# Kernel tuning notes

Measured on AMD Instinct MI355X. Metric: run time of the kernel, lower is better.

## Reference

```python
import jax, jax.numpy as jnp
import numpy as np

N, D, E, L, NL = 100000, 64, 400000, 4, 10000
NEG = jnp.float32(-1e30)


def _make_graph(key):
    k1, k2, k3, k4 = jax.random.split(key, 4)
    ncov = N - NL
    # nodes [0, NL) never appear as source -> exactly NL leaves
    src_cov = jnp.arange(ncov, dtype=jnp.int32) + NL
    src_rand = jax.random.randint(k1, (E - ncov,), NL, N, dtype=jnp.int32)
    src = jnp.concatenate([src_cov, src_rand])
    dst = jax.random.randint(k2, (E,), 0, N, dtype=jnp.int32)
    edge_index = jnp.stack([src, dst])  # [2, E]
    edge_attr = jax.random.normal(k3, (E, D), jnp.float32)
    # partition edges into L 'topological level' masks
    edge_masks = (jnp.arange(E) % L)[None, :] == jnp.arange(L)[:, None]  # [L, E] bool
    x = jax.random.normal(k4, (N, D), jnp.float32)
    return x, edge_index, edge_attr, edge_masks


def setup_inputs() -> dict:
    key = jax.random.key(0)
    kg1, kg2, kp = jax.random.split(key, 3)
    x1, ei1, ea1, em1 = _make_graph(kg1)
    x2, ei2, ea2, em2 = _make_graph(kg2)
    ks = jax.random.split(kp, 10)
    s = 1.0 / np.sqrt(D)
    params = {
        'We': jax.random.normal(ks[0], (D, D), jnp.float32) * s,
        'be': jax.random.normal(ks[1], (D,), jnp.float32) * s,
        'Wa': jax.random.normal(ks[2], (1, 2 * D), jnp.float32) * s,
        'ba': jax.random.normal(ks[3], (1,), jnp.float32) * s,
        'Wih': jax.random.normal(ks[4], (3 * D, D), jnp.float32) * s,
        'Whh': jax.random.normal(ks[5], (3 * D, D), jnp.float32) * s,
        'bih': jax.random.normal(ks[6], (3 * D,), jnp.float32) * s,
        'bhh': jax.random.normal(ks[7], (3 * D,), jnp.float32) * s,
        'Wc': jax.random.normal(ks[8], (2 * D, 2 * D), jnp.float32) * s,
        'bc': jax.random.normal(ks[9], (2 * D,), jnp.float32) * s,
    }
    return dict(x1=x1, edge_index1=ei1, edge_attr1=ea1, edge_masks1=em1,
                x2=x2, edge_index2=ei2, edge_attr2=ea2, edge_masks2=em2,
                **params, n_leaf=NL)


def _gru(x, h, Wih, Whh, bih, bhh):
    # torch.nn.GRUCell math
    gi = x @ Wih.T + bih
    gh = h @ Whh.T + bhh
    ir, iz, in_ = jnp.split(gi, 3, axis=-1)
    hr, hz, hn = jnp.split(gh, 3, axis=-1)
    r = jax.nn.sigmoid(ir + hr)
    z = jax.nn.sigmoid(iz + hz)
    n = jnp.tanh(in_ + r * hn)
    return (1.0 - z) * n + z * h


def _flow_forward(x, edge_index, edge_attr, edge_masks,
                  We, be, Wa, ba, Wih, Whh, bih, bhh):
    Nn, Dm = x.shape
    src, dst = edge_index[0], edge_index[1]
    root = jnp.ones((Nn,), bool).at[dst].set(False)  # nodes with no incoming edge
    eemb = edge_attr @ We.T + be                     # [E, D] edge_lin
    # roots: GRU with zero hidden; others start at 0 (zeros_like in torch)
    h0 = jnp.where(root[:, None], _gru(x, jnp.zeros_like(x), Wih, Whh, bih, bhh), 0.0)
    q = x[dst]                                       # h_prev_i, level-invariant

    def step(h, mask):
        k = h[src] + eemb                            # h_j + edge_emb
        logit = (jnp.concatenate([q, k], axis=-1) @ Wa.T + ba)[:, 0]  # [E]
        ml = jnp.where(mask, logit, NEG)
        mx = jnp.maximum(jax.ops.segment_max(ml, dst, num_segments=Nn), NEG)
        ex = jnp.where(mask, jnp.exp(ml - mx[dst]), 0.0)  # scatter-softmax numerator
        den = jax.ops.segment_sum(ex, dst, num_segments=Nn)
        alpha = ex / (den[dst] + 1e-16)
        msg = jax.ops.segment_sum(alpha[:, None] * h[src], dst, num_segments=Nn)
        nm = jax.ops.segment_sum(mask.astype(jnp.float32), dst, num_segments=Nn) > 0
        h_new = _gru(x, msg, Wih, Whh, bih, bhh)     # input=h_prev, hidden=msg
        return jnp.where(nm[:, None], h_new, h), None

    h, _ = jax.lax.scan(step, h0, edge_masks)
    return h


def reference(x1, edge_index1, edge_attr1, edge_masks1,
              x2, edge_index2, edge_attr2, edge_masks2,
              We, be, Wa, ba, Wih, Whh, bih, bhh, Wc, bc, n_leaf):
    o1 = _flow_forward(x1, edge_index1, edge_attr1, edge_masks1,
                       We, be, Wa, ba, Wih, Whh, bih, bhh)
    o2 = _flow_forward(x2, edge_index2, edge_attr2, edge_masks2,
                       We, be, Wa, ba, Wih, Whh, bih, bhh)
    Dm = x1.shape[1]
    leaf1 = jnp.ones((x1.shape[0],), bool).at[edge_index1[0]].set(False)
    leaf2 = jnp.ones((x2.shape[0],), bool).at[edge_index2[0]].set(False)
    idx1 = jnp.nonzero(leaf1, size=n_leaf)[0]
    idx2 = jnp.nonzero(leaf2, size=n_leaf)[0]
    feat = jnp.concatenate([o1[idx1], o2[idx2]], axis=-1) @ Wc.T + bc  # [NL, 2D]
    o1 = o1.at[idx1].set(feat[:, :Dm])
    o2 = o2.at[idx2].set(feat[:, Dm:])
    return (o1, o2)
```

## Files before the change

### kernel.cpp

```cpp
#include <hip/hip_runtime.h>

#define NN 100000
#define DD 64
#define EE 400000
#define LL 4
#define NLEAF 10000
#define NT (2*NN)
#define ETOT (2*EE)
#define M4 (4*NT)
#define NBLK ((M4 + 1023)/1024)

typedef __attribute__((ext_vector_type(8))) short bf8v;
typedef __attribute__((ext_vector_type(4))) float f4v;
typedef __attribute__((ext_vector_type(8))) unsigned short su8;

__device__ __forceinline__ float rcp_(float x){ return __builtin_amdgcn_rcpf(x); }
__device__ __forceinline__ float sigm_(float x){ return rcp_(1.f + __expf(-x)); }
__device__ __forceinline__ float tanh_(float x){
  x = fminf(fmaxf(x, -15.f), 15.f);
  float a = __expf(2.f*x);
  return (a - 1.f) * rcp_(a + 1.f);
}
__device__ __forceinline__ float wave_sum(float p){
  #pragma unroll
  for (int m = 1; m < 64; m <<= 1) p += __shfl_xor(p, m, 64);
  return p;
}
__device__ __forceinline__ unsigned short f2b(float f){
  union { float f; unsigned int u; } v; v.f = f;
  unsigned int r = v.u + 0x7FFF + ((v.u >> 16) & 1);
  return (unsigned short)(r >> 16);
}
__device__ __forceinline__ float b2f(unsigned short b){
  union { unsigned int u; float f; } v; v.u = ((unsigned int)b) << 16;
  return v.f;
}
__device__ __forceinline__ int cnt_at(const unsigned int* pcnt, int i){
  int l = i / NT; int td = i - l*NT;
  return (int)((pcnt[td] >> (8*l)) & 255u);
}

__global__ void k_init(unsigned int* __restrict__ pcnt, int* __restrict__ wlcnt,
                       int* __restrict__ row_ptr,
                       float* __restrict__ vvec, float* __restrict__ c0v,
                       unsigned short* __restrict__ whh_bf,
                       unsigned short* __restrict__ wih_bf,
                       const float* __restrict__ We, const float* __restrict__ Wa,
                       const float* __restrict__ be, const float* __restrict__ Whh,
                       const float* __restrict__ Wih) {
  int tid = blockIdx.x*blockDim.x + threadIdx.x;
  int stride = gridDim.x*blockDim.x;
  for (int i = tid; i < NT; i += stride) pcnt[i] = 0u;
  for (int i = tid; i < 192*64; i += stride) whh_bf[i] = f2b(Whh[i]);
  for (int i = tid; i < 208*64; i += stride) {
    int n = i >> 6, k = i & 63;
    unsigned short v;
    if (n < 192)       v = f2b(Wih[i]);
    else if (n == 192) v = f2b(Wa[k]);
    else               v = 0;
    wih_bf[i] = v;
  }
  if (blockIdx.x == 0 && threadIdx.x < 64) {
    int c = threadIdx.x;
    float acc = 0.f;
    for (int d = 0; d < 64; ++d) acc += We[d*64 + c] * Wa[64 + d];
    vvec[c] = acc;
    float p = wave_sum(be[c] * Wa[64 + c]);
    if (c == 0) { c0v[0] = p; row_ptr[M4] = ETOT; }
    if (c < 8) wlcnt[c] = 0;
  }
}

__global__ __launch_bounds__(256) void k_edot(
    const float* __restrict__ ea1, const float* __restrict__ ea2,
    const int* __restrict__ ei1, const int* __restrict__ ei2,
    const float* __restrict__ vvec, const float* __restrict__ c0v,
    float* __restrict__ edot, unsigned int* __restrict__ pcnt,
    unsigned char* __restrict__ rank8) {
  int lane = threadIdx.x & 63;
  int wave = blockIdx.x*(blockDim.x>>6) + (threadIdx.x>>6);
  int nw = gridDim.x*(blockDim.x>>6);
  int grp = lane >> 4, l16 = lane & 15;
  float4 v4 = ((const float4*)vvec)[l16];
  float c0 = c0v[0];
  const int NIT = ETOT/16;
  for (int it = wave; it < NIT; it += 2*nw) {
    int it2 = it + nw;
    bool hasB = (it2 < NIT);
    int e0 = it*16 + grp;
    int g = e0 >= EE;
    const float* ea = g ? ea2 : ea1;
    long eb = e0 - (long)g*EE;
    float4 a0 = ((const float4*)(ea + (eb     )*64))[l16];
    float4 a1 = ((const float4*)(ea + (eb +  4)*64))[l16];
    float4 a2 = ((const float4*)(ea + (eb +  8)*64))[l16];
    float4 a3 = ((const float4*)(ea + (eb + 12)*64))[l16];
    float4 b0, b1, b2, b3; int e1 = 0;
    if (hasB) {
      e1 = it2*16 + grp;
      int g2 = e1 >= EE;
      const float* eb2 = g2 ? ea2 : ea1;
      long ebb = e1 - (long)g2*EE;
      b0 = ((const float4*)(eb2 + (ebb     )*64))[l16];
      b1 = ((const float4*)(eb2 + (ebb +  4)*64))[l16];
      b2 = ((const float4*)(eb2 + (ebb +  8)*64))[l16];
      b3 = ((const float4*)(eb2 + (ebb + 12)*64))[l16];
    } else {
      b0 = b1 = b2 = b3 = make_float4(0.f,0.f,0.f,0.f);
    }
    float p0 = a0.x*v4.x + a0.y*v4.y + a0.z*v4.z + a0.w*v4.w;
    float p1 = a1.x*v4.x + a1.y*v4.y + a1.z*v4.z + a1.w*v4.w;
    float p2 = a2.x*v4.x + a2.y*v4.y + a2.z*v4.z + a2.w*v4.w;
    float p3 = a3.x*v4.x + a3.y*v4.y + a3.z*v4.z + a3.w*v4.w;
    float q0 = b0.x*v4.x + b0.y*v4.y + b0.z*v4.z + b0.w*v4.w;
    float q1 = b1.x*v4.x + b1.y*v4.y + b1.z*v4.z + b1.w*v4.w;
    float q2 = b2.x*v4.x + b2.y*v4.y + b2.z*v4.z + b2.w*v4.w;
    float q3 = b3.x*v4.x + b3.y*v4.y + b3.z*v4.z + b3.w*v4.w;
    #pragma unroll
    for (int m = 1; m < 16; m <<= 1) {
      p0 += __shfl_xor(p0, m, 64); p1 += __shfl_xor(p1, m, 64);
      p2 += __shfl_xor(p2, m, 64); p3 += __shfl_xor(p3, m, 64);
      q0 += __shfl_xor(q0, m, 64); q1 += __shfl_xor(q1, m, 64);
      q2 += __shfl_xor(q2, m, 64); q3 += __shfl_xor(q3, m, 64);
    }
    if (l16 == 0) {
      edot[e0]      = p0 + c0;
      edot[e0 +  4] = p1 + c0;
      edot[e0 +  8] = p2 + c0;
      edot[e0 + 12] = p3 + c0;
      if (hasB) {
        edot[e1]      = q0 + c0;
        edot[e1 +  4] = q1 + c0;
        edot[e1 +  8] = q2 + c0;
        edot[e1 + 12] = q3 + c0;
      }
    }
  }
  int tid = blockIdx.x*blockDim.x + threadIdx.x;
  int stride = gridDim.x*blockDim.x;
  for (int ee = tid; ee < ETOT; ee += stride) {
    int g = ee >= EE;
    int e = ee - g*EE;
    const int* ei = g ? ei2 : ei1;
    int d = ei[EE + e];
    int l = e & 3;
    unsigned old = atomicAdd(&pcnt[g*NN + d], 1u << (8*l));
    rank8[ee] = (unsigned char)((old >> (8*l)) & 255u);
  }
}

__global__ __launch_bounds__(256) void k_scan1(const unsigned int* __restrict__ pcnt,
                                               int* __restrict__ row_ptr,
                                               int2* __restrict__ partials) {
  __shared__ int ts[256];
  __shared__ int tsI[256];
  int tx = threadIdx.x;
  int base = blockIdx.x*1024 + tx*4;
  int v[4]; int s = 0, si = 0;
  #pragma unroll
  for (int u = 0; u < 4; ++u) {
    v[u] = (base+u < M4) ? cnt_at(pcnt, base+u) : 0;
    s += v[u]; si += (v[u] > 0);
  }
  ts[tx] = s; tsI[tx] = si; __syncthreads();
  for (int off = 1; off < 256; off <<= 1) {
    int t  = (tx >= off) ? ts[tx-off]  : 0;
    int ti = (tx >= off) ? tsI[tx-off] : 0;
    __syncthreads();
    ts[tx] += t; tsI[tx] += ti;
    __syncthreads();
  }
  int excl = ts[tx] - s;
  #pragma unroll
  for (int u = 0; u < 4; ++u) {
    if (base+u < M4) row_ptr[base+u] = excl;
    excl += v[u];
  }
  if (tx == 255) partials[blockIdx.x] = make_int2(ts[255], tsI[255]);
}

__global__ __launch_bounds__(256) void k_scan2(int2* __restrict__ partials) {
  __shared__ int tsx[256];
  __shared__ int tsy[256];
  int tx = threadIdx.x;
  int cx = 0, cy = 0;
  for (int base = 0; base < NBLK; base += 256) {
    int i = base + tx;
    int2 v = (i < NBLK) ? partials[i] : make_int2(0, 0);
    tsx[tx] = v.x; tsy[tx] = v.y; __syncthreads();
    for (int off = 1; off < 256; off <<= 1) {
      int ax = (tx >= off) ? tsx[tx-off] : 0;
      int ay = (tx >= off) ? tsy[tx-off] : 0;
      __syncthreads();
      tsx[tx] += ax; tsy[tx] += ay;
      __syncthreads();
    }
    int ix = tsx[tx], iy = tsy[tx];
    int tox = tsx[255], toy = tsy[255];
    __syncthreads();
    if (i < NBLK) partials[i] = make_int2(ix - v.x + cx, iy - v.y + cy);
    cx += tox; cy += toy;
  }
}

__global__ __launch_bounds__(256) void k_scan3(int* __restrict__ row_ptr,
                                               const int2* __restrict__ partials,
                                               const unsigned int* __restrict__ pcnt,
                                               int2* __restrict__ wl2,
                                               int* __restrict__ wlr,
                                               int* __restrict__ wlcnt,
                                               int* __restrict__ wlstart,
                                               int* __restrict__ lastlvl,
                                               int* __restrict__ vf) {
  __shared__ int ts[256];
  __shared__ int rootcnt;
  __shared__ int rootbase;
  int tx = threadIdx.x;
  if (tx == 0) rootcnt = 0;
  __syncthreads();
  int tdl = blockIdx.x*blockDim.x + threadIdx.x;
  int rootrank = -1;
  if (tdl < NT) {
    unsigned pv = pcnt[tdl];
    int ll = -1;
    if      (pv & 0xFF000000u) ll = 3;
    else if (pv & 0x00FF0000u) ll = 2;
    else if (pv & 0x0000FF00u) ll = 1;
    else if (pv & 0x000000FFu) ll = 0;
    lastlvl[tdl] = ll;
    int fl = 4;
    if      (pv & 0x000000FFu) fl = 0;
    else if (pv & 0x0000FF00u) fl = 1;
    else if (pv & 0x00FF0000u) fl = 2;
    else if (pv & 0xFF000000u) fl = 3;
    vf[tdl] = (ll < 0) ? 0 : fl + 1;
    if (ll < 0) rootrank = atomicAdd(&rootcnt, 1);
  }
  int base = blockIdx.x*1024 + tx*4;
  int2 add = partials[blockIdx.x];
  int indv[4]; int rpv[4]; int si = 0;
  #pragma unroll
  for (int u = 0; u < 4; ++u) {
    int i = base + u;
    indv[u] = 0; rpv[u] = 0;
    if (i < M4) {
      rpv[u] = row_ptr[i] + add.x;
      row_ptr[i] = rpv[u];
      indv[u] = cnt_at(pcnt, i) > 0;
    }
    si += indv[u];
  }
  ts[tx] = si; __syncthreads();
  for (int off = 1; off < 256; off <<= 1) {
    int t2 = (tx >= off) ? ts[tx-off] : 0;
    __syncthreads();
    ts[tx] += t2;
    __syncthreads();
  }
  int gpos = add.y + ts[tx] - si;
  #pragma unroll
  for (int u = 0; u < 4; ++u) {
    int i = base + u;
    if (i < M4) {
      int l = i / NT;
      if (i - l*NT == 0) wlstart[l] = gpos;
      if (indv[u]) wl2[gpos] = make_int2(i - l*NT, rpv[u]);
      if (i == M4 - 1) {
        wlstart[4] = gpos + indv[u];
        wl2[gpos + indv[u]] = make_int2(0, ETOT);
      }
      gpos += indv[u];
    }
  }
  __syncthreads();
  if (tx == 0 && rootcnt > 0) rootbase = atomicAdd(&wlcnt[4], rootcnt);
  __syncthreads();
  if (rootrank >= 0) wlr[rootbase + rootrank] = tdl;
}

__global__ __launch_bounds__(256) void k_fillgix(
    const int* __restrict__ ei1, const int* __restrict__ ei2,
    const float* __restrict__ edot, const float* __restrict__ ba,
    const int* __restrict__ row_ptr, const unsigned char* __restrict__ rank8,
    const int* __restrict__ vf,
    int2* __restrict__ csr,
    const float* __restrict__ x1, const float* __restrict__ x2,
    const unsigned short* __restrict__ wih_bf,
    const float* __restrict__ bih,
    ushort2* __restrict__ gi01, unsigned short* __restrict__ gi2p,
    float* __restrict__ xdot) {
  {
    int tid = blockIdx.x*blockDim.x + threadIdx.x;
    int stride = gridDim.x*blockDim.x;
    float bav = ba[0];
    for (int ee = tid; ee < ETOT; ee += stride) {
      int g = ee >= EE;
      int e = ee - g*EE;
      const int* ei = g ? ei2 : ei1;
      int s = ei[e], d = ei[EE + e];
      int l = e & 3;
      int td = g*NN + d;
      int gs = g*NN + s;
      int pos = row_ptr[l*NT + td] + (int)rank8[ee];
      csr[pos] = make_int2((vf[gs] << 24) | gs, __float_as_int(edot[ee] + bav));
    }
  }
  int lane = threadIdx.x & 63, w = threadIdx.x >> 6;
  int l15 = lane & 15, quad = lane >> 4;
  int wave = blockIdx.x*4 + w, nw = gridDim.x*4;
  float bi0[4], bi1[4], bi2[4];
  #pragma unroll
  for (int tt = 0; tt < 4; ++tt) {
    int f = l15 + 16*tt;
    bi0[tt]=bih[f]; bi1[tt]=bih[64+f]; bi2[tt]=bih[128+f];
  }
  for (int tl = wave; tl < NT/16; tl += nw) {
    int ta = tl*16 + l15;
    const float* xp = (ta < NN) ? x1 + (size_t)ta*64 : x2 + (size_t)(ta-NN)*64;
    float4 v0 = ((const float4*)xp)[quad*2];
    float4 v1 = ((const float4*)xp)[quad*2 + 1];
    float4 v2 = ((const float4*)xp)[quad*2 + 8];
    float4 v3 = ((const float4*)xp)[quad*2 + 9];
    bf8v a0, a1;
    a0[0]=(short)f2b(v0.x); a0[1]=(short)f2b(v0.y); a0[2]=(short)f2b(v0.z); a0[3]=(short)f2b(v0.w);
    a0[4]=(short)f2b(v1.x); a0[5]=(short)f2b(v1.y); a0[6]=(short)f2b(v1.z); a0[7]=(short)f2b(v1.w);
    a1[0]=(short)f2b(v2.x); a1[1]=(short)f2b(v2.y); a1[2]=(short)f2b(v2.z); a1[3]=(short)f2b(v2.w);
    a1[4]=(short)f2b(v3.x); a1[5]=(short)f2b(v3.y); a1[6]=(short)f2b(v3.z); a1[7]=(short)f2b(v3.w);
    f4v acc[13];
    #pragma unroll
    for (int nt = 0; nt < 13; ++nt) {
      bf8v b0 = *(const bf8v*)&wih_bf[(nt*16 + l15)*64 + quad*8];
      bf8v b1 = *(const bf8v*)&wih_bf[(nt*16 + l15)*64 + 32 + quad*8];
      f4v z = {0.f, 0.f, 0.f, 0.f};
      z = __builtin_amdgcn_mfma_f32_16x16x32_bf16(a0, b0, z, 0, 0, 0);
      acc[nt] = __builtin_amdgcn_mfma_f32_16x16x32_bf16(a1, b1, z, 0, 0, 0);
    }
    #pragma unroll
    for (int r = 0; r < 4; ++r) {
      int t = tl*16 + quad*4 + r;
      #pragma unroll
      for (int tt = 0; tt < 4; ++tt) {
        int f = tt*16 + l15;
        ushort2 p; p.x = f2b(acc[tt][r] + bi0[tt]); p.y = f2b(acc[tt+4][r] + bi1[tt]);
        gi01[(size_t)t*64 + f] = p;
        gi2p[(size_t)t*64 + f] = f2b(acc[tt+8][r] + bi2[tt]);
      }
      if (l15 == 0) xdot[t] = acc[12][r];
    }
  }
}

__global__ __launch_bounds__(256) void k_roots(
    const ushort2* __restrict__ gi01, const unsigned short* __restrict__ gi2p,
    const float* __restrict__ bhh, const float* __restrict__ Wa,
    const int* __restrict__ wlr, const int* __restrict__ wlcnt,
    float* __restrict__ hout, unsigned short* __restrict__ hbf,
    float* __restrict__ hdot) {
  int l16 = threadIdx.x & 15;
  int grp = (blockIdx.x*blockDim.x + threadIdx.x) >> 4;
  int ngrp = (gridDim.x*blockDim.x) >> 4;
  int cnt = wlcnt[4];
  float bh0[4], bh1[4], bh2[4], wk[4];
  #pragma unroll
  for (int j = 0; j < 4; ++j) {
    int f = l16*4 + j;
    bh0[j]=bhh[f]; bh1[j]=bhh[64+f]; bh2[j]=bhh[128+f]; wk[j]=Wa[64+f];
  }
  for (int i = grp; i < cnt; i += ngrp) {
    int t = wlr[i];
    float hds = 0.f;
    #pragma unroll
    for (int j = 0; j < 4; ++j) {
      int f = l16*4 + j;
      ushort2 p01 = gi01[(size_t)t*64 + f];
      float g2 = b2f(gi2p[(size_t)t*64 + f]);
      float rr = sigm_(b2f(p01.x) + bh0[j]);
      float zz = sigm_(b2f(p01.y) + bh1[j]);
      float nn = tanh_(g2 + rr*bh2[j]);
      float hv = (1.f - zz)*nn;
      hout[(size_t)t*64 + f] = hv;
      hbf[(size_t)t*64 + f] = f2b(hv);
      hds += hv * wk[j];
    }
    hds += __shfl_xor(hds, 1, 64);
    hds += __shfl_xor(hds, 2, 64);
    hds += __shfl_xor(hds, 4, 64);
    hds += __shfl_xor(hds, 8, 64);
    if (l16 == 0) hdot[t] = hds;
  }
}

__global__ void k_msg(const int2* __restrict__ csr,
                      const float* __restrict__ xdot,
                      const float* __restrict__ hdot, const unsigned short* __restrict__ hbf,
                      const int2* __restrict__ wl2, const int* __restrict__ wlstart,
                      int level, unsigned short* __restrict__ msgn_bf) {
  int l8 = threadIdx.x & 7;
  int grp = (blockIdx.x*blockDim.x + threadIdx.x) >> 3;
  int ngrp = (gridDim.x*blockDim.x) >> 3;
  int start = wlstart[level];
  int cnt = wlstart[level+1] - start;
  for (int i = grp; i < cnt; i += ngrp) {
    int2 eA = wl2[start + i];
    int p1 = wl2[start + i + 1].y;
    int t = eA.x;
    int p0 = eA.y;
    float xd = xdot[t];
    float den = 0.f;
    float m0=0.f, m1=0.f, m2=0.f, m3=0.f, m4=0.f, m5=0.f, m6=0.f, m7=0.f;
    int p = p0;
    for (; p + 2 <= p1; p += 2) {
      int2 prA = csr[p];
      int2 prB = csr[p+1];
      int sA = prA.x & 0x00FFFFFF;
      int sB = prB.x & 0x00FFFFFF;
      bool hA = (prA.x >> 24) <= level;
      bool hB = (prB.x >> 24) <= level;
      float hdA = hA ? hdot[sA] : 0.f;
      float hdB = hB ? hdot[sB] : 0.f;
      su8 h8A = {0,0,0,0,0,0,0,0}, h8B = {0,0,0,0,0,0,0,0};
      if (hA) h8A = *(const su8*)(hbf + (size_t)sA*64 + l8*8);
      if (hB) h8B = *(const su8*)(hbf + (size_t)sB*64 + l8*8);
      float wvA = __expf(xd + hdA + __int_as_float(prA.y));
      float wvB = __expf(xd + hdB + __int_as_float(prB.y));
      den += wvA + wvB;
      m0 += wvA*b2f(h8A[0]) + wvB*b2f(h8B[0]);
      m1 += wvA*b2f(h8A[1]) + wvB*b2f(h8B[1]);
      m2 += wvA*b2f(h8A[2]) + wvB*b2f(h8B[2]);
      m3 += wvA*b2f(h8A[3]) + wvB*b2f(h8B[3]);
      m4 += wvA*b2f(h8A[4]) + wvB*b2f(h8B[4]);
      m5 += wvA*b2f(h8A[5]) + wvB*b2f(h8B[5]);
      m6 += wvA*b2f(h8A[6]) + wvB*b2f(h8B[6]);
      m7 += wvA*b2f(h8A[7]) + wvB*b2f(h8B[7]);
    }
    if (p < p1) {
      int2 pr = csr[p];
      int s = pr.x & 0x00FFFFFF;
      bool hv = (pr.x >> 24) <= level;
      float hd = hv ? hdot[s] : 0.f;
      float wv = __expf(xd + hd + __int_as_float(pr.y));
      den += wv;
      if (hv) {
        su8 h8 = *(const su8*)(hbf + (size_t)s*64 + l8*8);
        m0 += wv*b2f(h8[0]); m1 += wv*b2f(h8[1]);
        m2 += wv*b2f(h8[2]); m3 += wv*b2f(h8[3]);
        m4 += wv*b2f(h8[4]); m5 += wv*b2f(h8[5]);
        m6 += wv*b2f(h8[6]); m7 += wv*b2f(h8[7]);
      }
    }
    float rd = rcp_(den + 1e-16f);
    su8 o;
    o[0] = f2b(m0*rd); o[1] = f2b(m1*rd); o[2] = f2b(m2*rd); o[3] = f2b(m3*rd);
    o[4] = f2b(m4*rd); o[5] = f2b(m5*rd); o[6] = f2b(m6*rd); o[7] = f2b(m7*rd);
    *(su8*)(msgn_bf + (long)i*64 + l8*8) = o;
  }
}

__global__ __launch_bounds__(256) void k_gru(
    const unsigned short* __restrict__ whh_bf, const float* __restrict__ bhh,
    const float* __restrict__ Wa,
    const ushort2* __restrict__ gi01, const unsigned short* __restrict__ gi2p,
    const int2* __restrict__ wl2, const int* __restrict__ wlstart,
    const int* __restrict__ lastlvl, int level,
    const unsigned short* __restrict__ msgn_bf,
    float* __restrict__ hout, unsigned short* __restrict__ hbf,
    float* __restrict__ hdot) {
  int lane = threadIdx.x & 63, w = threadIdx.x >> 6;
  int l15 = lane & 15, quad = lane >> 4;
  int start = wlstart[level];
  int cnt = wlstart[level+1] - start;
  int ntile = (cnt + 15) >> 4;
  int wave = blockIdx.x*4 + w, nw = gridDim.x*4;
  float bh0[4], bh1[4], bh2[4], wk4[4];
  #pragma unroll
  for (int tt = 0; tt < 4; ++tt) {
    int f = tt*16 + l15;
    bh0[tt]=bhh[f]; bh1[tt]=bhh[64+f]; bh2[tt]=bhh[128+f];
    wk4[tt]=Wa[64+f];
  }
  for (int tl = wave; tl < ntile; tl += nw) {
    int base = tl*16;
    long abase = (long)(base + l15)*64;
    bf8v a0 = *(const bf8v*)&msgn_bf[abase + quad*8];
    bf8v a1 = *(const bf8v*)&msgn_bf[abase + 32 + quad*8];
    f4v acc[12];
    #pragma unroll
    for (int nt = 0; nt < 12; ++nt) {
      bf8v b0 = *(const bf8v*)&whh_bf[(nt*16 + l15)*64 + quad*8];
      bf8v b1 = *(const bf8v*)&whh_bf[(nt*16 + l15)*64 + 32 + quad*8];
      f4v z = {0.f, 0.f, 0.f, 0.f};
      z = __builtin_amdgcn_mfma_f32_16x16x32_bf16(a0, b0, z, 0, 0, 0);
      acc[nt] = __builtin_amdgcn_mfma_f32_16x16x32_bf16(a1, b1, z, 0, 0, 0);
    }
    #pragma unroll
    for (int r = 0; r < 4; ++r) {
      int i = base + quad*4 + r;
      if (i < cnt) {
        int t = wl2[start + i].x;
        int ll = lastlvl[t];
        float hds = 0.f;
        #pragma unroll
        for (int tt = 0; tt < 4; ++tt) {
          int f = tt*16 + l15;
          ushort2 p01 = gi01[(size_t)t*64 + f];
          float g2v = b2f(gi2p[(size_t)t*64 + f]);
          float mv  = b2f(msgn_bf[(long)i*64 + f]);
          float rr = sigm_(b2f(p01.x) + acc[tt][r]   + bh0[tt]);
          float zz = sigm_(b2f(p01.y) + acc[tt+4][r] + bh1[tt]);
          float nn = tanh_(g2v + rr*(acc[tt+8][r] + bh2[tt]));
          float hv = (1.f - zz)*nn + zz*mv;
          if (ll == level) hout[(size_t)t*64 + f] = hv;
          if (level < 3)  hbf[(size_t)t*64 + f] = f2b(hv);
          hds += hv * wk4[tt];
        }
        if (level < 3) {
          hds += __shfl_xor(hds, 1, 64);
          hds += __shfl_xor(hds, 2, 64);
          hds += __shfl_xor(hds, 4, 64);
          hds += __shfl_xor(hds, 8, 64);
          if (l15 == 0) hdot[t] = hds;
        }
      }
    }
  }
}

__global__ __launch_bounds__(256) void k_final(const float* __restrict__ Wc,
                                               const float* __restrict__ bc,
                                               float* __restrict__ hout) {
  __shared__ float WT[128*128];
  for (int idx = threadIdx.x; idx < 128*128; idx += 256) {
    int j = idx >> 7, c = idx & 127;
    WT[c*128 + j] = Wc[idx];
  }
  __syncthreads();
  int lane = threadIdx.x & 63, w = threadIdx.x >> 6;
  int wave = blockIdx.x*4 + w, nw = gridDim.x*4;
  float bc0 = bc[lane], bc1 = bc[64 + lane];
  for (int i = wave; i < NLEAF; i += nw) {
    float h1v = hout[(long)i*64 + lane];
    float h2v = hout[(long)(NN + i)*64 + lane];
    float acc0 = 0.f, acc1 = 0.f;
    for (int c = 0; c < 64; ++c) {
      float m1 = __shfl(h1v, c, 64);
      float m2 = __shfl(h2v, c, 64);
      acc0 += WT[c*128 + lane]      * m1 + WT[(64+c)*128 + lane]      * m2;
      acc1 += WT[c*128 + 64 + lane] * m1 + WT[(64+c)*128 + 64 + lane] * m2;
    }
    hout[(long)i*64 + lane]        = acc0 + bc0;
    hout[(long)(NN + i)*64 + lane] = acc1 + bc1;
  }
}

extern "C" void kernel_launch(void* const* d_in, const int* in_sizes, int n_in,
                              void* d_out, int out_size, void* d_ws, size_t ws_size,
                              hipStream_t stream) {
  const float* x1  = (const float*)d_in[0];
  const int*   ei1 = (const int*)  d_in[1];
  const float* ea1 = (const float*)d_in[2];
  const float* x2  = (const float*)d_in[4];
  const int*   ei2 = (const int*)  d_in[5];
  const float* ea2 = (const float*)d_in[6];
  const float* We  = (const float*)d_in[8];
  const float* be  = (const float*)d_in[9];
  const float* Wa  = (const float*)d_in[10];
  const float* ba  = (const float*)d_in[11];
  const float* Wih = (const float*)d_in[12];
  const float* Whh = (const float*)d_in[13];
  const float* bih = (const float*)d_in[14];
  const float* bhh = (const float*)d_in[15];
  const float* Wc  = (const float*)d_in[16];
  const float* bc  = (const float*)d_in[17];
  float* hout = (float*)d_out;

  float* f = (float*)d_ws;
  ushort2* gi01 = (ushort2*)f;        f += (size_t)NT*64;
  unsigned short* gi2p    = (unsigned short*)f;  f += (size_t)NT*32;
  unsigned short* msgn_bf = (unsigned short*)f;  f += (size_t)NT*32;
  unsigned short* hbf     = (unsigned short*)f;  f += (size_t)NT*32;
  unsigned short* whh_bf  = (unsigned short*)f;  f += 8192;
  unsigned short* wih_bf  = (unsigned short*)f;  f += 8192;
  float* edot = f;  f += ETOT;
  float* xdot = f;  f += NT;
  float* hdot = f;  f += NT;
  float* vvec = f;  f += 64;
  float* c0v  = f;  f += 64;
  int2* csr     = (int2*)f; f += (size_t)2*ETOT;
  unsigned int* pcnt = (unsigned int*)f;  f += NT;
  int* row_ptr  = (int*)f;  f += (M4 + 64);
  int* lastlvl  = (int*)f;  f += NT;
  int* vf       = (int*)f;  f += NT;
  int2* wl2     = (int2*)f; f += (size_t)2*(M4 + 64);
  int* wlr      = (int*)f;  f += NT;
  int* wlcnt    = (int*)f;  f += 64;
  int* wlstart  = (int*)f;  f += 64;
  int2* partials = (int2*)f; f += 2048;
  unsigned char* rank8 = (unsigned char*)f;  f += ETOT/4;

  k_init <<<dim3(512),  dim3(256), 0, stream>>>(pcnt, wlcnt, row_ptr, vvec, c0v, whh_bf, wih_bf, We, Wa, be, Whh, Wih);
  k_edot <<<dim3(2048), dim3(256), 0, stream>>>(ea1, ea2, ei1, ei2, vvec, c0v, edot, pcnt, rank8);
  k_scan1<<<dim3(NBLK), dim3(256), 0, stream>>>(pcnt, row_ptr, partials);
  k_scan2<<<dim3(1),    dim3(256), 0, stream>>>(partials);
  k_scan3<<<dim3(NBLK), dim3(256), 0, stream>>>(row_ptr, partials, pcnt, wl2, wlr, wlcnt, wlstart, lastlvl, vf);
  k_fillgix<<<dim3(2048), dim3(256), 0, stream>>>(ei1, ei2, edot, ba, row_ptr, rank8, vf, csr, x1, x2, wih_bf, bih, gi01, gi2p, xdot);
  k_roots<<<dim3(256), dim3(256), 0, stream>>>(gi01, gi2p, bhh, Wa, wlr, wlcnt, hout, hbf, hdot);
  for (int l = 0; l < 4; ++l) {
    k_msg<<<dim3(4096), dim3(256), 0, stream>>>(csr, xdot, hdot, hbf, wl2, wlstart, l, msgn_bf);
    k_gru<<<dim3(2048), dim3(256), 0, stream>>>(whh_bf, bhh, Wa, gi01, gi2p, wl2, wlstart, lastlvl, l, msgn_bf, hout, hbf, hdot);
  }
  k_final<<<dim3(640), dim3(256), 0, stream>>>(Wc, bc, hout);
}
```

Measured before the change: 509.7 us.

## Drop per-node xdot term from softmax and widen k_msg lanes to 16 features

The attention logit's destination-node term (x·Wa) is constant within each destination's softmax, so it cancels. The change removes it, along with the extra MFMA tile that computed it, the xdot buffer and its per-node read in k_msg. k_msg now uses 4 lanes per destination with 16 features each instead of 8 lanes with 8, halving the redundant csr, hdot and exp work per edge. The risks are higher register use, wider per-lane gathers, and exp overflow without the shift (softmax here is not max-stabilised).

```diff
diff --git a/kernel.cpp b/kernel.cpp
--- a/kernel.cpp
+++ b/kernel.cpp
@@ -52,14 +52,7 @@
   int stride = gridDim.x*blockDim.x;
   for (int i = tid; i < NT; i += stride) pcnt[i] = 0u;
   for (int i = tid; i < 192*64; i += stride) whh_bf[i] = f2b(Whh[i]);
-  for (int i = tid; i < 208*64; i += stride) {
-    int n = i >> 6, k = i & 63;
-    unsigned short v;
-    if (n < 192)       v = f2b(Wih[i]);
-    else if (n == 192) v = f2b(Wa[k]);
-    else               v = 0;
-    wih_bf[i] = v;
-  }
+  for (int i = tid; i < 192*64; i += stride) wih_bf[i] = f2b(Wih[i]);
   if (blockIdx.x == 0 && threadIdx.x < 64) {
     int c = threadIdx.x;
     float acc = 0.f;
@@ -287,8 +280,7 @@
     const float* __restrict__ x1, const float* __restrict__ x2,
     const unsigned short* __restrict__ wih_bf,
     const float* __restrict__ bih,
-    ushort2* __restrict__ gi01, unsigned short* __restrict__ gi2p,
-    float* __restrict__ xdot) {
+    ushort2* __restrict__ gi01, unsigned short* __restrict__ gi2p) {
   {
     int tid = blockIdx.x*blockDim.x + threadIdx.x;
     int stride = gridDim.x*blockDim.x;
@@ -326,26 +318,29 @@
     a0[4]=(short)f2b(v1.x); a0[5]=(short)f2b(v1.y); a0[6]=(short)f2b(v1.z); a0[7]=(short)f2b(v1.w);
     a1[0]=(short)f2b(v2.x); a1[1]=(short)f2b(v2.y); a1[2]=(short)f2b(v2.z); a1[3]=(short)f2b(v2.w);
     a1[4]=(short)f2b(v3.x); a1[5]=(short)f2b(v3.y); a1[6]=(short)f2b(v3.z); a1[7]=(short)f2b(v3.w);
-    f4v acc[13];
     #pragma unroll
-    for (int nt = 0; nt < 13; ++nt) {
-      bf8v b0 = *(const bf8v*)&wih_bf[(nt*16 + l15)*64 + quad*8];
-      bf8v b1 = *(const bf8v*)&wih_bf[(nt*16 + l15)*64 + 32 + quad*8];
-      f4v z = {0.f, 0.f, 0.f, 0.f};
-      z = __builtin_amdgcn_mfma_f32_16x16x32_bf16(a0, b0, z, 0, 0, 0);
-      acc[nt] = __builtin_amdgcn_mfma_f32_16x16x32_bf16(a1, b1, z, 0, 0, 0);
-    }
-    #pragma unroll
-    for (int r = 0; r < 4; ++r) {
-      int t = tl*16 + quad*4 + r;
+    for (int tt = 0; tt < 4; ++tt) {
+      bf8v bR0 = *(const bf8v*)&wih_bf[((tt  )*16 + l15)*64 + quad*8];
+      bf8v bR1 = *(const bf8v*)&wih_bf[((tt  )*16 + l15)*64 + 32 + quad*8];
+      bf8v bZ0 = *(const bf8v*)&wih_bf[((tt+4)*16 + l15)*64 + quad*8];
+      bf8v bZ1 = *(const bf8v*)&wih_bf[((tt+4)*16 + l15)*64 + 32 + quad*8];
+      bf8v bN0 = *(const bf8v*)&wih_bf[((tt+8)*16 + l15)*64 + quad*8];
+      bf8v bN1 = *(const bf8v*)&wih_bf[((tt+8)*16 + l15)*64 + 32 + quad*8];
+      f4v zR = {0.f,0.f,0.f,0.f}, zZ = {0.f,0.f,0.f,0.f}, zN = {0.f,0.f,0.f,0.f};
+      zR = __builtin_amdgcn_mfma_f32_16x16x32_bf16(a0, bR0, zR, 0, 0, 0);
+      zR = __builtin_amdgcn_mfma_f32_16x16x32_bf16(a1, bR1, zR, 0, 0, 0);
+      zZ = __builtin_amdgcn_mfma_f32_16x16x32_bf16(a0, bZ0, zZ, 0, 0, 0);
+      zZ = __builtin_amdgcn_mfma_f32_16x16x32_bf16(a1, bZ1, zZ, 0, 0, 0);
+      zN = __builtin_amdgcn_mfma_f32_16x16x32_bf16(a0, bN0, zN, 0, 0, 0);
+      zN = __builtin_amdgcn_mfma_f32_16x16x32_bf16(a1, bN1, zN, 0, 0, 0);
+      int f = tt*16 + l15;
       #pragma unroll
-      for (int tt = 0; tt < 4; ++tt) {
-        int f = tt*16 + l15;
-        ushort2 p; p.x = f2b(acc[tt][r] + bi0[tt]); p.y = f2b(acc[tt+4][r] + bi1[tt]);
+      for (int r = 0; r < 4; ++r) {
+        int t = tl*16 + quad*4 + r;
+        ushort2 p; p.x = f2b(zR[r] + bi0[tt]); p.y = f2b(zZ[r] + bi1[tt]);
         gi01[(size_t)t*64 + f] = p;
-        gi2p[(size_t)t*64 + f] = f2b(acc[tt+8][r] + bi2[tt]);
-      }
-      if (l15 == 0) xdot[t] = acc[12][r];
+        gi2p[(size_t)t*64 + f] = f2b(zN[r] + bi2[tt]);
+      }
     }
   }
 }
@@ -391,23 +386,22 @@
 }
 
 __global__ void k_msg(const int2* __restrict__ csr,
-                      const float* __restrict__ xdot,
                       const float* __restrict__ hdot, const unsigned short* __restrict__ hbf,
                       const int2* __restrict__ wl2, const int* __restrict__ wlstart,
                       int level, unsigned short* __restrict__ msgn_bf) {
-  int l8 = threadIdx.x & 7;
-  int grp = (blockIdx.x*blockDim.x + threadIdx.x) >> 3;
-  int ngrp = (gridDim.x*blockDim.x) >> 3;
+  int l4 = threadIdx.x & 3;
+  int grp = (blockIdx.x*blockDim.x + threadIdx.x) >> 2;
+  int ngrp = (gridDim.x*blockDim.x) >> 2;
   int start = wlstart[level];
   int cnt = wlstart[level+1] - start;
   for (int i = grp; i < cnt; i += ngrp) {
     int2 eA = wl2[start + i];
     int p1 = wl2[start + i + 1].y;
-    int t = eA.x;
     int p0 = eA.y;
-    float xd = xdot[t];
     float den = 0.f;
-    float m0=0.f, m1=0.f, m2=0.f, m3=0.f, m4=0.f, m5=0.f, m6=0.f, m7=0.f;
+    float m[16];
+    #pragma unroll
+    for (int j = 0; j < 16; ++j) m[j] = 0.f;
     int p = p0;
     for (; p + 2 <= p1; p += 2) {
       int2 prA = csr[p];
@@ -418,41 +412,51 @@
       bool hB = (prB.x >> 24) <= level;
       float hdA = hA ? hdot[sA] : 0.f;
       float hdB = hB ? hdot[sB] : 0.f;
-      su8 h8A = {0,0,0,0,0,0,0,0}, h8B = {0,0,0,0,0,0,0,0};
-      if (hA) h8A = *(const su8*)(hbf + (size_t)sA*64 + l8*8);
-      if (hB) h8B = *(const su8*)(hbf + (size_t)sB*64 + l8*8);
-      float wvA = __expf(xd + hdA + __int_as_float(prA.y));
-      float wvB = __expf(xd + hdB + __int_as_float(prB.y));
+      su8 a0 = {0,0,0,0,0,0,0,0}, a1 = {0,0,0,0,0,0,0,0};
+      su8 b0 = {0,0,0,0,0,0,0,0}, b1 = {0,0,0,0,0,0,0,0};
+      if (hA) {
+        a0 = *(const su8*)(hbf + (size_t)sA*64 + l4*16);
+        a1 = *(const su8*)(hbf + (size_t)sA*64 + l4*16 + 8);
+      }
+      if (hB) {
+        b0 = *(const su8*)(hbf + (size_t)sB*64 + l4*16);
+        b1 = *(const su8*)(hbf + (size_t)sB*64 + l4*16 + 8);
+      }
+      float wvA = __expf(hdA + __int_as_float(prA.y));
+      float wvB = __expf(hdB + __int_as_float(prB.y));
       den += wvA + wvB;
-      m0 += wvA*b2f(h8A[0]) + wvB*b2f(h8B[0]);
-      m1 += wvA*b2f(h8A[1]) + wvB*b2f(h8B[1]);
-      m2 += wvA*b2f(h8A[2]) + wvB*b2f(h8B[2]);
-      m3 += wvA*b2f(h8A[3]) + wvB*b2f(h8B[3]);
-      m4 += wvA*b2f(h8A[4]) + wvB*b2f(h8B[4]);
-      m5 += wvA*b2f(h8A[5]) + wvB*b2f(h8B[5]);
-      m6 += wvA*b2f(h8A[6]) + wvB*b2f(h8B[6]);
-      m7 += wvA*b2f(h8A[7]) + wvB*b2f(h8B[7]);
+      #pragma unroll
+      for (int j = 0; j < 8; ++j) {
+        m[j]   += wvA*b2f(a0[j]) + wvB*b2f(b0[j]);
+        m[8+j] += wvA*b2f(a1[j]) + wvB*b2f(b1[j]);
+      }
     }
     if (p < p1) {
       int2 pr = csr[p];
       int s = pr.x & 0x00FFFFFF;
       bool hv = (pr.x >> 24) <= level;
       float hd = hv ? hdot[s] : 0.f;
-      float wv = __expf(xd + hd + __int_as_float(pr.y));
+      float wv = __expf(hd + __int_as_float(pr.y));
       den += wv;
       if (hv) {
-        su8 h8 = *(const su8*)(hbf + (size_t)s*64 + l8*8);
-        m0 += wv*b2f(h8[0]); m1 += wv*b2f(h8[1]);
-        m2 += wv*b2f(h8[2]); m3 += wv*b2f(h8[3]);
-        m4 += wv*b2f(h8[4]); m5 += wv*b2f(h8[5]);
-        m6 += wv*b2f(h8[6]); m7 += wv*b2f(h8[7]);
+        su8 a0 = *(const su8*)(hbf + (size_t)s*64 + l4*16);
+        su8 a1 = *(const su8*)(hbf + (size_t)s*64 + l4*16 + 8);
+        #pragma unroll
+        for (int j = 0; j < 8; ++j) {
+          m[j]   += wv*b2f(a0[j]);
+          m[8+j] += wv*b2f(a1[j]);
+        }
       }
     }
     float rd = rcp_(den + 1e-16f);
-    su8 o;
-    o[0] = f2b(m0*rd); o[1] = f2b(m1*rd); o[2] = f2b(m2*rd); o[3] = f2b(m3*rd);
-    o[4] = f2b(m4*rd); o[5] = f2b(m5*rd); o[6] = f2b(m6*rd); o[7] = f2b(m7*rd);
-    *(su8*)(msgn_bf + (long)i*64 + l8*8) = o;
+    su8 o0, o1;
+    #pragma unroll
+    for (int j = 0; j < 8; ++j) {
+      o0[j] = f2b(m[j]*rd);
+      o1[j] = f2b(m[8+j]*rd);
+    }
+    *(su8*)(msgn_bf + (long)i*64 + l4*16)     = o0;
+    *(su8*)(msgn_bf + (long)i*64 + l4*16 + 8) = o1;
   }
 }
 
@@ -581,7 +585,6 @@
   unsigned short* whh_bf  = (unsigned short*)f;  f += 8192;
   unsigned short* wih_bf  = (unsigned short*)f;  f += 8192;
   float* edot = f;  f += ETOT;
-  float* xdot = f;  f += NT;
   float* hdot = f;  f += NT;
   float* vvec = f;  f += 64;
   float* c0v  = f;  f += 64;
@@ -602,10 +605,10 @@
   k_scan1<<<dim3(NBLK), dim3(256), 0, stream>>>(pcnt, row_ptr, partials);
   k_scan2<<<dim3(1),    dim3(256), 0, stream>>>(partials);
   k_scan3<<<dim3(NBLK), dim3(256), 0, stream>>>(row_ptr, partials, pcnt, wl2, wlr, wlcnt, wlstart, lastlvl, vf);
-  k_fillgix<<<dim3(2048), dim3(256), 0, stream>>>(ei1, ei2, edot, ba, row_ptr, rank8, vf, csr, x1, x2, wih_bf, bih, gi01, gi2p, xdot);
+  k_fillgix<<<dim3(2048), dim3(256), 0, stream>>>(ei1, ei2, edot, ba, row_ptr, rank8, vf, csr, x1, x2, wih_bf, bih, gi01, gi2p);
   k_roots<<<dim3(256), dim3(256), 0, stream>>>(gi01, gi2p, bhh, Wa, wlr, wlcnt, hout, hbf, hdot);
   for (int l = 0; l < 4; ++l) {
-    k_msg<<<dim3(4096), dim3(256), 0, stream>>>(csr, xdot, hdot, hbf, wl2, wlstart, l, msgn_bf);
+    k_msg<<<dim3(4096), dim3(256), 0, stream>>>(csr, hdot, hbf, wl2, wlstart, l, msgn_bf);
     k_gru<<<dim3(2048), dim3(256), 0, stream>>>(whh_bf, bhh, Wa, gi01, gi2p, wl2, wlstart, lastlvl, l, msgn_bf, hout, hbf, hdot);
   }
   k_final<<<dim3(640), dim3(256), 0, stream>>>(Wc, bc, hout);
```

Result: no change. 501.7 us (-1.6%).
